# Kernel optimization log

Hardware: AMD Instinct MI355X
Metric: run time of the kernel (lower is better)

## Reference

```python
import jax, jax.numpy as jnp
import numpy as np

D_MODEL = 1024
N_HEADS = 16
LN_EPS = 1e-6  # flax LayerNorm default

def setup_inputs() -> dict:
    key = jax.random.key(0)
    k1, k2, k3 = jax.random.split(key, 3)
    B, S = 2, 2048
    x = jax.random.normal(k1, (B, S, D_MODEL), dtype=jnp.float32)
    W_qkv = jax.random.normal(k2, (D_MODEL, 3 * D_MODEL), dtype=jnp.float32) / np.sqrt(D_MODEL)
    W_out = jax.random.normal(k3, (D_MODEL, D_MODEL), dtype=jnp.float32) / np.sqrt(D_MODEL)
    q_scale = jnp.ones((D_MODEL,), dtype=jnp.float32)
    k_scale = jnp.ones((D_MODEL,), dtype=jnp.float32)
    return {"x": x, "W_qkv": W_qkv, "q_scale": q_scale, "k_scale": k_scale, "W_out": W_out}

def _layernorm(t, scale):
    mu = jnp.mean(t, axis=-1, keepdims=True)
    var = jnp.var(t, axis=-1, keepdims=True)
    return (t - mu) * jax.lax.rsqrt(var + LN_EPS) * scale

def reference(x, W_qkv, q_scale, k_scale, W_out):
    B, S, D = x.shape
    H = N_HEADS
    Hd = D // H
    # fused QKV projection (no bias)
    qkv = jnp.einsum('bsd,de->bse', x, W_qkv)
    q, k, v = jnp.split(qkv, 3, axis=-1)
    # QK-LayerNorm over full d_model (before head split), scale only
    q = _layernorm(q, q_scale)
    k = _layernorm(k, k_scale)
    # split heads: [b, s, h, hd]
    q = q.reshape(B, S, H, Hd)
    k = k.reshape(B, S, H, Hd)
    v = v.reshape(B, S, H, Hd)
    # eager attention with causal mask
    scores = jnp.einsum('bshd,bthd->bhst', q / jnp.sqrt(Hd).astype(q.dtype), k)  # [b,h,s,t]
    future = jnp.triu(jnp.ones((S, S), dtype=bool), 1)  # True on strictly-future positions
    scores = jnp.where(future[None, None, :, :], jnp.finfo(scores.dtype).min, scores)
    attn = jax.nn.softmax(scores, axis=-1)
    ctx = jnp.einsum('bhst,bthd->bshd', attn, v)
    out = jnp.einsum('bsd,de->bse', ctx.reshape(B, S, D), W_out)
    return out
```

## Files before the change

kernel.cpp:

```cpp
#include <hip/hip_runtime.h>
#include <cstdint>
#include <cstddef>

typedef __attribute__((ext_vector_type(8))) short short8;
typedef __attribute__((ext_vector_type(4))) float floatx4;

__device__ __forceinline__ float bf2f(unsigned short u) {
  union { unsigned int i; float f; } c; c.i = ((unsigned int)u) << 16; return c.f;
}
__device__ __forceinline__ unsigned short f2bf(float f) {
  union { float f; unsigned int i; } c; c.f = f;
  unsigned int r = c.i + 0x7fffu + ((c.i >> 16) & 1u);
  return (unsigned short)(r >> 16);
}
__device__ __forceinline__ unsigned short f2bf_trunc(float f) {
  union { float f; unsigned int i; } c; c.f = f;
  return (unsigned short)(c.i >> 16);
}

__device__ __forceinline__ void glds16(const unsigned short* g, unsigned short* l) {
  __builtin_amdgcn_global_load_lds((const __attribute__((address_space(1))) void*)g,
                                   (__attribute__((address_space(3))) void*)l, 16, 0, 0);
}

__global__ __launch_bounds__(256) void k_cvt(const float* __restrict__ in,
                                             unsigned short* __restrict__ out, int n4) {
  int i = blockIdx.x * 256 + threadIdx.x;
  if (i >= n4) return;
  float4 v = ((const float4*)in)[i];
  ushort4 o = { f2bf(v.x), f2bf(v.y), f2bf(v.z), f2bf(v.w) };
  ((ushort4*)out)[i] = o;
}

__global__ __launch_bounds__(1024) void k_transpose_cvt(const float* __restrict__ in,
                                                        unsigned short* __restrict__ out,
                                                        int R, int C) {
  __shared__ unsigned short t[32][33];
  int c = blockIdx.x * 32 + threadIdx.x;
  int r = blockIdx.y * 32 + threadIdx.y;
  t[threadIdx.y][threadIdx.x] = f2bf(in[(size_t)r * C + c]);
  __syncthreads();
  int oc = blockIdx.y * 32 + threadIdx.x;
  int orow = blockIdx.x * 32 + threadIdx.y;
  out[(size_t)orow * R + oc] = t[threadIdx.x][threadIdx.y];
}

__global__ __launch_bounds__(1024) void k_transpose_v(const unsigned short* __restrict__ qkv,
                                                      unsigned short* __restrict__ VT) {
  int bh = blockIdx.z, b = bh >> 4, h = bh & 15;
  __shared__ unsigned short t[32][33];
  int hd = blockIdx.x * 32 + threadIdx.x;
  int s  = blockIdx.y * 32 + threadIdx.y;
  t[threadIdx.y][threadIdx.x] = qkv[(size_t)(b * 2048 + s) * 3072 + 2048 + h * 64 + hd];
  __syncthreads();
  int os  = blockIdx.y * 32 + threadIdx.x;
  int ohd = blockIdx.x * 32 + threadIdx.y;
  VT[((size_t)bh * 64 + ohd) * 2048 + os] = t[threadIdx.x][threadIdx.y];
}

template <int MT, bool F32OUT>
__global__ __launch_bounds__(256) void k_gemm_bt(const unsigned short* __restrict__ A,
                                                 const unsigned short* __restrict__ BT,
                                                 void* __restrict__ Cout,
                                                 int M, int N, int K) {
  constexpr int NI = MT / 32;
  __shared__ unsigned short As[MT * 32];
  __shared__ unsigned short Bs[128 * 32];
  const int bm = blockIdx.x * MT, bn = blockIdx.y * 128;
  const int tid = threadIdx.x;
  const int wave = tid >> 6, lane = tid & 63;
  const int wm = (wave & 1) * (MT / 2), wn = (wave >> 1) * 64;
  const int lrow = lane & 15, lgrp = lane >> 4;
  floatx4 acc[NI][4] = {};

  const int lr4 = lane >> 2, lc8 = (lane & 3) * 8;
  const int br0 = wave * 32;
  const unsigned short* Bg0 = BT + (size_t)(bn + br0 + lr4) * K + lc8;
  const unsigned short* Bg1 = BT + (size_t)(bn + br0 + 16 + lr4) * K + lc8;
  unsigned short* lB0 = &Bs[br0 * 32];
  unsigned short* lB1 = &Bs[(br0 + 16) * 32];
  const int ar0 = wave * (MT / 4);
  const unsigned short* Ag0 = A + (size_t)(bm + ar0 + lr4) * K + lc8;
  const unsigned short* Ag1 = A + (size_t)(bm + ar0 + 16 + lr4) * K + lc8;
  unsigned short* lA0 = &As[ar0 * 32];
  unsigned short* lA1 = &As[(ar0 + 16) * 32];

  for (int k0 = 0; k0 < K; k0 += 32) {
    glds16(Ag0 + k0, lA0);
    if (MT == 128) glds16(Ag1 + k0, lA1);
    glds16(Bg0 + k0, lB0);
    glds16(Bg1 + k0, lB1);
    __syncthreads();
    short8 a[NI], bfr[4];
#pragma unroll
    for (int i = 0; i < NI; ++i)
      a[i] = *(const short8*)&As[(wm + i * 16 + lrow) * 32 + lgrp * 8];
#pragma unroll
    for (int j = 0; j < 4; ++j)
      bfr[j] = *(const short8*)&Bs[(wn + j * 16 + lrow) * 32 + lgrp * 8];
#pragma unroll
    for (int i = 0; i < NI; ++i)
#pragma unroll
      for (int j = 0; j < 4; ++j)
        acc[i][j] = __builtin_amdgcn_mfma_f32_16x16x32_bf16(a[i], bfr[j], acc[i][j], 0, 0, 0);
    __syncthreads();
  }
#pragma unroll
  for (int i = 0; i < NI; ++i)
#pragma unroll
    for (int j = 0; j < 4; ++j)
#pragma unroll
      for (int r = 0; r < 4; ++r) {
        int m = bm + wm + i * 16 + lgrp * 4 + r;
        int n = bn + wn + j * 16 + lrow;
        if (F32OUT)
          ((float*)Cout)[(size_t)m * N + n] = acc[i][j][r];
        else
          ((unsigned short*)Cout)[(size_t)m * N + n] = f2bf(acc[i][j][r]);
      }
}

__global__ __launch_bounds__(256) void k_ln(const unsigned short* __restrict__ qkv,
                                            const float* __restrict__ q_scale,
                                            const float* __restrict__ k_scale,
                                            unsigned short* __restrict__ q_n,
                                            unsigned short* __restrict__ k_n) {
  const int tok = blockIdx.x;
  const int tid = threadIdx.x, wave = tid >> 6, lane = tid & 63;
  __shared__ float red[2][4];
  const unsigned short* row = qkv + (size_t)tok * 3072;
#pragma unroll
  for (int seg = 0; seg < 2; ++seg) {
    const unsigned short* p  = row + seg * 1024;
    const float* sc = seg ? k_scale : q_scale;
    unsigned short* outp = (seg ? k_n : q_n) + (size_t)tok * 1024;
    ushort4 u = *(const ushort4*)&p[tid * 4];
    float xv[4] = { bf2f(u.x), bf2f(u.y), bf2f(u.z), bf2f(u.w) };
    float sum = xv[0] + xv[1] + xv[2] + xv[3];
    float sq  = xv[0]*xv[0] + xv[1]*xv[1] + xv[2]*xv[2] + xv[3]*xv[3];
    for (int off = 32; off; off >>= 1) {
      sum += __shfl_down(sum, off, 64);
      sq  += __shfl_down(sq,  off, 64);
    }
    if (lane == 0) { red[0][wave] = sum; red[1][wave] = sq; }
    __syncthreads();
    sum = red[0][0] + red[0][1] + red[0][2] + red[0][3];
    sq  = red[1][0] + red[1][1] + red[1][2] + red[1][3];
    __syncthreads();
    float mean = sum * (1.0f / 1024.0f);
    float var  = sq * (1.0f / 1024.0f) - mean * mean;
    float rstd = rsqrtf(var + 1e-6f);
    if (seg == 0) rstd *= 0.18033688011112042f;
    float4 su = *(const float4*)&sc[tid * 4];
    ushort4 o;
    o.x = f2bf((xv[0] - mean) * rstd * su.x);
    o.y = f2bf((xv[1] - mean) * rstd * su.y);
    o.z = f2bf((xv[2] - mean) * rstd * su.z);
    o.w = f2bf((xv[3] - mean) * rstd * su.w);
    *(ushort4*)&outp[tid * 4] = o;
  }
}

template <int TB, bool MASKED>
__device__ __forceinline__ void attn_tile(int t0, int q0w,
    const short8 qa0, const short8 qa1,
    const unsigned short* Ks, const unsigned short* Vs, unsigned short* Psw,
    floatx4 (&o)[4], float (&l_i)[4], int lrow, int lgrp) {
  floatx4 sc[TB];
#pragma unroll
  for (int tb = 0; tb < TB; ++tb) {
    floatx4 z = {};
    short8 kb0 = *(const short8*)&Ks[(tb * 16 + lrow) * 72 + lgrp * 8];
    z = __builtin_amdgcn_mfma_f32_16x16x32_bf16(qa0, kb0, z, 0, 0, 0);
    short8 kb1 = *(const short8*)&Ks[(tb * 16 + lrow) * 72 + 32 + lgrp * 8];
    z = __builtin_amdgcn_mfma_f32_16x16x32_bf16(qa1, kb1, z, 0, 0, 0);
    sc[tb] = z;
  }
#pragma unroll
  for (int r = 0; r < 4; ++r) {
    const int qr = q0w + lgrp * 4 + r;
#pragma unroll
    for (int tb = 0; tb < TB; ++tb) {
      float p = exp2f(sc[tb][r]);
      if (MASKED) p = (t0 + tb * 16 + lrow <= qr) ? p : 0.0f;
      unsigned short us = f2bf_trunc(p);
      l_i[r] += bf2f(us);
      Psw[(lgrp * 4 + r) * 136 + tb * 16 + lrow] = us;
    }
  }
#pragma unroll
  for (int kk = 0; kk < TB / 2; ++kk) {
    short8 pa = *(const short8*)&Psw[lrow * 136 + kk * 32 + lgrp * 8];
#pragma unroll
    for (int nb = 0; nb < 4; ++nb) {
      short8 vb = *(const short8*)&Vs[(nb * 16 + lrow) * 136 + kk * 32 + lgrp * 8];
      o[nb] = __builtin_amdgcn_mfma_f32_16x16x32_bf16(pa, vb, o[nb], 0, 0, 0);
    }
  }
}

__global__ __launch_bounds__(256) void k_flash(const unsigned short* __restrict__ q_n,
                                               const unsigned short* __restrict__ k_n,
                                               const unsigned short* __restrict__ VT,
                                               unsigned short* __restrict__ ctx) {
  const int S = 2048, D = 1024;
  const int bh = blockIdx.x, b = bh >> 4, h = bh & 15;
  const int qt = 31 - (int)blockIdx.y;
  const int q0 = qt * 64;
  const int tid = threadIdx.x, wave = tid >> 6, lane = tid & 63;
  const int lrow = lane & 15, lgrp = lane >> 4;
  __shared__ unsigned short Ks[128 * 72];
  __shared__ unsigned short Vs[64 * 136];
  __shared__ unsigned short Ps[4][16 * 136];
  unsigned short* Psw = Ps[wave];

  const unsigned short* kg = k_n + (size_t)(b * S) * D + h * 64;
  const unsigned short* vg = VT + (size_t)bh * 64 * S;
  const int ksr = tid >> 3, ksc = (tid & 7) * 8;
  const int vsr = tid >> 4, vsc = (tid & 15) * 8;

  const int q0w = q0 + wave * 16;
  const unsigned short* qp = q_n + (size_t)(b * S + q0w + lrow) * D + h * 64;
  const short8 qa0 = *(const short8*)(qp + lgrp * 8);
  const short8 qa1 = *(const short8*)(qp + 32 + lgrp * 8);
  floatx4 o[4] = {};
  float l_i[4] = {};

  const int tend = q0 + 64;
  for (int t0 = 0; t0 < tend; t0 += 128) {
#pragma unroll
    for (int j = 0; j < 4; ++j) {
      int r = ksr + j * 32;
      *(int4*)&Ks[r * 72 + ksc] = *(const int4*)(kg + (size_t)(t0 + r) * D + ksc);
    }
#pragma unroll
    for (int j = 0; j < 4; ++j) {
      int r = vsr + j * 16;
      *(int4*)&Vs[r * 136 + vsc] = *(const int4*)(vg + (size_t)r * S + t0 + vsc);
    }
    __syncthreads();
    if (t0 + 128 <= q0)
      attn_tile<8, false>(t0, q0w, qa0, qa1, Ks, Vs, Psw, o, l_i, lrow, lgrp);
    else if (tend - t0 >= 128)
      attn_tile<8, true>(t0, q0w, qa0, qa1, Ks, Vs, Psw, o, l_i, lrow, lgrp);
    else
      attn_tile<4, true>(t0, q0w, qa0, qa1, Ks, Vs, Psw, o, l_i, lrow, lgrp);
    __syncthreads();
  }

  float inv[4];
#pragma unroll
  for (int r = 0; r < 4; ++r) {
    float l = l_i[r];
#pragma unroll
    for (int off = 1; off < 16; off <<= 1) l += __shfl_xor(l, off, 64);
    inv[r] = 1.0f / l;
  }
  unsigned short* op = ctx + (size_t)(b * S + q0w) * D + h * 64;
#pragma unroll
  for (int nb = 0; nb < 4; ++nb)
#pragma unroll
    for (int r = 0; r < 4; ++r) {
      int row = lgrp * 4 + r;
      op[(size_t)row * D + nb * 16 + lrow] = f2bf(o[nb][r] * inv[r]);
    }
}

extern "C" void kernel_launch(void* const* d_in, const int* in_sizes, int n_in,
                              void* d_out, int out_size, void* d_ws, size_t ws_size,
                              hipStream_t stream) {
  const float* x       = (const float*)d_in[0];
  const float* W_qkv   = (const float*)d_in[1];
  const float* q_scale = (const float*)d_in[2];
  const float* k_scale = (const float*)d_in[3];
  const float* W_out   = (const float*)d_in[4];
  float* out = (float*)d_out;
  char* ws = (char*)d_ws;
  unsigned short* WT_qkv = (unsigned short*)(ws + 0);
  unsigned short* WT_out = (unsigned short*)(ws + 6291456);
  unsigned short* qkv    = (unsigned short*)(ws + 8388608);
  unsigned short* q_nb   = (unsigned short*)(ws + 33554432);
  unsigned short* k_nb   = (unsigned short*)(ws + 41943040);
  unsigned short* VT     = (unsigned short*)(ws + 50331648);
  unsigned short* x_bf   = (unsigned short*)(ws + 58720256);
  unsigned short* ctx    = qkv;

  k_cvt<<<4096, 256, 0, stream>>>(x, x_bf, 4096 * 1024 / 4);
  k_transpose_cvt<<<dim3(96, 32), dim3(32, 32), 0, stream>>>(W_qkv, WT_qkv, 1024, 3072);
  k_transpose_cvt<<<dim3(32, 32), dim3(32, 32), 0, stream>>>(W_out, WT_out, 1024, 1024);
  k_gemm_bt<128, false><<<dim3(32, 24), 256, 0, stream>>>(x_bf, WT_qkv, qkv, 4096, 3072, 1024);
  k_ln<<<4096, 256, 0, stream>>>(qkv, q_scale, k_scale, q_nb, k_nb);
  k_transpose_v<<<dim3(2, 64, 32), dim3(32, 32), 0, stream>>>(qkv, VT);
  k_flash<<<dim3(32, 32), 256, 0, stream>>>(q_nb, k_nb, VT, ctx);
  k_gemm_bt<64, true><<<dim3(64, 8), 256, 0, stream>>>(ctx, WT_out, out, 4096, 1024, 1024);
}
```

Baseline: 208.8 us.

## Merge prep and LN/V-transpose launches; transpose score MFMA in flash attention

Three preprocessing kernels (x conversion and two weight transposes) become one k_prep launch, and the LayerNorm and V-transpose kernels become one k_lnv launch. The transposes now use 256-thread blocks instead of 1024. In flash attention, the QK^T MFMA operands are swapped so each lane holds four key positions for a single query. This allows vectorized ushort4 stores of P, a single running row sum with a shorter shuffle reduction, and round-to-nearest instead of truncation when converting P to bf16. The row sum now accumulates the unrounded fp32 p values while the stored P is rounded, which slightly changes numerics.

```diff
diff --git a/kernel.cpp b/kernel.cpp
--- a/kernel.cpp
+++ b/kernel.cpp
@@ -13,49 +13,46 @@
   unsigned int r = c.i + 0x7fffu + ((c.i >> 16) & 1u);
   return (unsigned short)(r >> 16);
 }
-__device__ __forceinline__ unsigned short f2bf_trunc(float f) {
-  union { float f; unsigned int i; } c; c.f = f;
-  return (unsigned short)(c.i >> 16);
-}
 
 __device__ __forceinline__ void glds16(const unsigned short* g, unsigned short* l) {
   __builtin_amdgcn_global_load_lds((const __attribute__((address_space(1))) void*)g,
                                    (__attribute__((address_space(3))) void*)l, 16, 0, 0);
 }
 
-__global__ __launch_bounds__(256) void k_cvt(const float* __restrict__ in,
-                                             unsigned short* __restrict__ out, int n4) {
-  int i = blockIdx.x * 256 + threadIdx.x;
-  if (i >= n4) return;
-  float4 v = ((const float4*)in)[i];
-  ushort4 o = { f2bf(v.x), f2bf(v.y), f2bf(v.z), f2bf(v.w) };
-  ((ushort4*)out)[i] = o;
-}
-
-__global__ __launch_bounds__(1024) void k_transpose_cvt(const float* __restrict__ in,
-                                                        unsigned short* __restrict__ out,
-                                                        int R, int C) {
+__device__ __forceinline__ void tr_tile(const float* __restrict__ in,
+                                        unsigned short* __restrict__ out,
+                                        int R, int C, int bx, int by, int tid,
+                                        unsigned short (*t)[33]) {
+  const int cx = tid & 31, rl = tid >> 5;
+#pragma unroll
+  for (int i = 0; i < 4; ++i)
+    t[rl + i * 8][cx] = f2bf(in[(size_t)(by * 32 + rl + i * 8) * C + bx * 32 + cx]);
+  __syncthreads();
+  const int oc = by * 32 + cx;
+#pragma unroll
+  for (int i = 0; i < 4; ++i)
+    out[(size_t)(bx * 32 + rl + i * 8) * R + oc] = t[cx][rl + i * 8];
+}
+
+__global__ __launch_bounds__(256) void k_prep(const float* __restrict__ x,
+                                              const float* __restrict__ Wq,
+                                              const float* __restrict__ Wo,
+                                              unsigned short* __restrict__ x_bf,
+                                              unsigned short* __restrict__ WTq,
+                                              unsigned short* __restrict__ WTo) {
   __shared__ unsigned short t[32][33];
-  int c = blockIdx.x * 32 + threadIdx.x;
-  int r = blockIdx.y * 32 + threadIdx.y;
-  t[threadIdx.y][threadIdx.x] = f2bf(in[(size_t)r * C + c]);
-  __syncthreads();
-  int oc = blockIdx.y * 32 + threadIdx.x;
-  int orow = blockIdx.x * 32 + threadIdx.y;
-  out[(size_t)orow * R + oc] = t[threadIdx.x][threadIdx.y];
-}
-
-__global__ __launch_bounds__(1024) void k_transpose_v(const unsigned short* __restrict__ qkv,
-                                                      unsigned short* __restrict__ VT) {
-  int bh = blockIdx.z, b = bh >> 4, h = bh & 15;
-  __shared__ unsigned short t[32][33];
-  int hd = blockIdx.x * 32 + threadIdx.x;
-  int s  = blockIdx.y * 32 + threadIdx.y;
-  t[threadIdx.y][threadIdx.x] = qkv[(size_t)(b * 2048 + s) * 3072 + 2048 + h * 64 + hd];
-  __syncthreads();
-  int os  = blockIdx.y * 32 + threadIdx.x;
-  int ohd = blockIdx.x * 32 + threadIdx.y;
-  VT[((size_t)bh * 64 + ohd) * 2048 + os] = t[threadIdx.x][threadIdx.y];
+  const int bid = blockIdx.x, tid = threadIdx.x;
+  if (bid < 3072) {
+    tr_tile(Wq, WTq, 1024, 3072, bid % 96, bid / 96, tid, t);
+  } else if (bid < 4096) {
+    int v = bid - 3072;
+    tr_tile(Wo, WTo, 1024, 1024, v & 31, v >> 5, tid, t);
+  } else {
+    int i = (bid - 4096) * 256 + tid;
+    float4 v = ((const float4*)x)[i];
+    ushort4 o = { f2bf(v.x), f2bf(v.y), f2bf(v.z), f2bf(v.w) };
+    ((ushort4*)x_bf)[i] = o;
+  }
 }
 
 template <int MT, bool F32OUT>
@@ -120,73 +117,88 @@
       }
 }
 
-__global__ __launch_bounds__(256) void k_ln(const unsigned short* __restrict__ qkv,
-                                            const float* __restrict__ q_scale,
-                                            const float* __restrict__ k_scale,
-                                            unsigned short* __restrict__ q_n,
-                                            unsigned short* __restrict__ k_n) {
-  const int tok = blockIdx.x;
-  const int tid = threadIdx.x, wave = tid >> 6, lane = tid & 63;
-  __shared__ float red[2][4];
-  const unsigned short* row = qkv + (size_t)tok * 3072;
-#pragma unroll
-  for (int seg = 0; seg < 2; ++seg) {
-    const unsigned short* p  = row + seg * 1024;
-    const float* sc = seg ? k_scale : q_scale;
-    unsigned short* outp = (seg ? k_n : q_n) + (size_t)tok * 1024;
-    ushort4 u = *(const ushort4*)&p[tid * 4];
-    float xv[4] = { bf2f(u.x), bf2f(u.y), bf2f(u.z), bf2f(u.w) };
-    float sum = xv[0] + xv[1] + xv[2] + xv[3];
-    float sq  = xv[0]*xv[0] + xv[1]*xv[1] + xv[2]*xv[2] + xv[3]*xv[3];
-    for (int off = 32; off; off >>= 1) {
-      sum += __shfl_down(sum, off, 64);
-      sq  += __shfl_down(sq,  off, 64);
-    }
-    if (lane == 0) { red[0][wave] = sum; red[1][wave] = sq; }
-    __syncthreads();
-    sum = red[0][0] + red[0][1] + red[0][2] + red[0][3];
-    sq  = red[1][0] + red[1][1] + red[1][2] + red[1][3];
-    __syncthreads();
-    float mean = sum * (1.0f / 1024.0f);
-    float var  = sq * (1.0f / 1024.0f) - mean * mean;
-    float rstd = rsqrtf(var + 1e-6f);
-    if (seg == 0) rstd *= 0.18033688011112042f;
-    float4 su = *(const float4*)&sc[tid * 4];
-    ushort4 o;
-    o.x = f2bf((xv[0] - mean) * rstd * su.x);
-    o.y = f2bf((xv[1] - mean) * rstd * su.y);
-    o.z = f2bf((xv[2] - mean) * rstd * su.z);
-    o.w = f2bf((xv[3] - mean) * rstd * su.w);
-    *(ushort4*)&outp[tid * 4] = o;
+__global__ __launch_bounds__(256) void k_lnv(const unsigned short* __restrict__ qkv,
+                                             const float* __restrict__ q_scale,
+                                             const float* __restrict__ k_scale,
+                                             unsigned short* __restrict__ q_n,
+                                             unsigned short* __restrict__ k_n,
+                                             unsigned short* __restrict__ VT) {
+  const int bid = blockIdx.x, tid = threadIdx.x;
+  if (bid < 4096) {
+    const int tok = bid;
+    const int wave = tid >> 6, lane = tid & 63;
+    __shared__ float red[2][4];
+    const unsigned short* row = qkv + (size_t)tok * 3072;
+#pragma unroll
+    for (int seg = 0; seg < 2; ++seg) {
+      const unsigned short* p  = row + seg * 1024;
+      const float* sc = seg ? k_scale : q_scale;
+      unsigned short* outp = (seg ? k_n : q_n) + (size_t)tok * 1024;
+      ushort4 u = *(const ushort4*)&p[tid * 4];
+      float xv[4] = { bf2f(u.x), bf2f(u.y), bf2f(u.z), bf2f(u.w) };
+      float sum = xv[0] + xv[1] + xv[2] + xv[3];
+      float sq  = xv[0]*xv[0] + xv[1]*xv[1] + xv[2]*xv[2] + xv[3]*xv[3];
+      for (int off = 32; off; off >>= 1) {
+        sum += __shfl_down(sum, off, 64);
+        sq  += __shfl_down(sq,  off, 64);
+      }
+      if (lane == 0) { red[0][wave] = sum; red[1][wave] = sq; }
+      __syncthreads();
+      sum = red[0][0] + red[0][1] + red[0][2] + red[0][3];
+      sq  = red[1][0] + red[1][1] + red[1][2] + red[1][3];
+      __syncthreads();
+      float mean = sum * (1.0f / 1024.0f);
+      float var  = sq * (1.0f / 1024.0f) - mean * mean;
+      float rstd = rsqrtf(var + 1e-6f);
+      if (seg == 0) rstd *= 0.18033688011112042f;
+      float4 su = *(const float4*)&sc[tid * 4];
+      ushort4 o;
+      o.x = f2bf((xv[0] - mean) * rstd * su.x);
+      o.y = f2bf((xv[1] - mean) * rstd * su.y);
+      o.z = f2bf((xv[2] - mean) * rstd * su.z);
+      o.w = f2bf((xv[3] - mean) * rstd * su.w);
+      *(ushort4*)&outp[tid * 4] = o;
+    }
+  } else {
+    __shared__ unsigned short t[32][33];
+    const int v = bid - 4096;
+    const int bh = v & 31, b = bh >> 4, h = bh & 15;
+    const int sy = (v >> 5) & 63, hx = v >> 11;
+    const int cx = tid & 31, rl = tid >> 5;
+#pragma unroll
+    for (int i = 0; i < 4; ++i)
+      t[rl + i * 8][cx] =
+        qkv[(size_t)(b * 2048 + sy * 32 + rl + i * 8) * 3072 + 2048 + h * 64 + hx * 32 + cx];
+    __syncthreads();
+#pragma unroll
+    for (int i = 0; i < 4; ++i)
+      VT[((size_t)bh * 64 + hx * 32 + rl + i * 8) * 2048 + sy * 32 + cx] = t[cx][rl + i * 8];
   }
 }
 
 template <int TB, bool MASKED>
-__device__ __forceinline__ void attn_tile(int t0, int q0w,
+__device__ __forceinline__ void attn_tile(int t0, int qcol,
     const short8 qa0, const short8 qa1,
     const unsigned short* Ks, const unsigned short* Vs, unsigned short* Psw,
-    floatx4 (&o)[4], float (&l_i)[4], int lrow, int lgrp) {
-  floatx4 sc[TB];
+    floatx4 (&o)[4], float& lsum, int lrow, int lgrp) {
 #pragma unroll
   for (int tb = 0; tb < TB; ++tb) {
-    floatx4 z = {};
+    floatx4 st = {};
     short8 kb0 = *(const short8*)&Ks[(tb * 16 + lrow) * 72 + lgrp * 8];
-    z = __builtin_amdgcn_mfma_f32_16x16x32_bf16(qa0, kb0, z, 0, 0, 0);
+    st = __builtin_amdgcn_mfma_f32_16x16x32_bf16(kb0, qa0, st, 0, 0, 0);
     short8 kb1 = *(const short8*)&Ks[(tb * 16 + lrow) * 72 + 32 + lgrp * 8];
-    z = __builtin_amdgcn_mfma_f32_16x16x32_bf16(qa1, kb1, z, 0, 0, 0);
-    sc[tb] = z;
-  }
-#pragma unroll
-  for (int r = 0; r < 4; ++r) {
-    const int qr = q0w + lgrp * 4 + r;
-#pragma unroll
-    for (int tb = 0; tb < TB; ++tb) {
-      float p = exp2f(sc[tb][r]);
-      if (MASKED) p = (t0 + tb * 16 + lrow <= qr) ? p : 0.0f;
-      unsigned short us = f2bf_trunc(p);
-      l_i[r] += bf2f(us);
-      Psw[(lgrp * 4 + r) * 136 + tb * 16 + lrow] = us;
-    }
+    st = __builtin_amdgcn_mfma_f32_16x16x32_bf16(kb1, qa1, st, 0, 0, 0);
+    ushort4 pu;
+    float ps = 0.0f;
+#pragma unroll
+    for (int r = 0; r < 4; ++r) {
+      float p = exp2f(st[r]);
+      if (MASKED) p = (t0 + tb * 16 + lgrp * 4 + r <= qcol) ? p : 0.0f;
+      ps += p;
+      ((unsigned short*)&pu)[r] = f2bf(p);
+    }
+    lsum += ps;
+    *(ushort4*)&Psw[lrow * 136 + tb * 16 + lgrp * 4] = pu;
   }
 #pragma unroll
   for (int kk = 0; kk < TB / 2; ++kk) {
@@ -220,11 +232,12 @@
   const int vsr = tid >> 4, vsc = (tid & 15) * 8;
 
   const int q0w = q0 + wave * 16;
-  const unsigned short* qp = q_n + (size_t)(b * S + q0w + lrow) * D + h * 64;
+  const int qcol = q0w + lrow;
+  const unsigned short* qp = q_n + (size_t)(b * S + qcol) * D + h * 64;
   const short8 qa0 = *(const short8*)(qp + lgrp * 8);
   const short8 qa1 = *(const short8*)(qp + 32 + lgrp * 8);
   floatx4 o[4] = {};
-  float l_i[4] = {};
+  float lsum = 0.0f;
 
   const int tend = q0 + 64;
   for (int t0 = 0; t0 < tend; t0 += 128) {
@@ -240,22 +253,20 @@
     }
     __syncthreads();
     if (t0 + 128 <= q0)
-      attn_tile<8, false>(t0, q0w, qa0, qa1, Ks, Vs, Psw, o, l_i, lrow, lgrp);
+      attn_tile<8, false>(t0, qcol, qa0, qa1, Ks, Vs, Psw, o, lsum, lrow, lgrp);
     else if (tend - t0 >= 128)
-      attn_tile<8, true>(t0, q0w, qa0, qa1, Ks, Vs, Psw, o, l_i, lrow, lgrp);
+      attn_tile<8, true>(t0, qcol, qa0, qa1, Ks, Vs, Psw, o, lsum, lrow, lgrp);
     else
-      attn_tile<4, true>(t0, q0w, qa0, qa1, Ks, Vs, Psw, o, l_i, lrow, lgrp);
-    __syncthreads();
-  }
-
+      attn_tile<4, true>(t0, qcol, qa0, qa1, Ks, Vs, Psw, o, lsum, lrow, lgrp);
+    __syncthreads();
+  }
+
+  lsum += __shfl_xor(lsum, 16, 64);
+  lsum += __shfl_xor(lsum, 32, 64);
   float inv[4];
 #pragma unroll
-  for (int r = 0; r < 4; ++r) {
-    float l = l_i[r];
-#pragma unroll
-    for (int off = 1; off < 16; off <<= 1) l += __shfl_xor(l, off, 64);
-    inv[r] = 1.0f / l;
-  }
+  for (int r = 0; r < 4; ++r)
+    inv[r] = 1.0f / __shfl(lsum, lgrp * 20 + r, 64);
   unsigned short* op = ctx + (size_t)(b * S + q0w) * D + h * 64;
 #pragma unroll
   for (int nb = 0; nb < 4; ++nb)
@@ -285,12 +296,9 @@
   unsigned short* x_bf   = (unsigned short*)(ws + 58720256);
   unsigned short* ctx    = qkv;
 
-  k_cvt<<<4096, 256, 0, stream>>>(x, x_bf, 4096 * 1024 / 4);
-  k_transpose_cvt<<<dim3(96, 32), dim3(32, 32), 0, stream>>>(W_qkv, WT_qkv, 1024, 3072);
-  k_transpose_cvt<<<dim3(32, 32), dim3(32, 32), 0, stream>>>(W_out, WT_out, 1024, 1024);
+  k_prep<<<8192, 256, 0, stream>>>(x, W_qkv, W_out, x_bf, WT_qkv, WT_out);
   k_gemm_bt<128, false><<<dim3(32, 24), 256, 0, stream>>>(x_bf, WT_qkv, qkv, 4096, 3072, 1024);
-  k_ln<<<4096, 256, 0, stream>>>(qkv, q_scale, k_scale, q_nb, k_nb);
-  k_transpose_v<<<dim3(2, 64, 32), dim3(32, 32), 0, stream>>>(qkv, VT);
+  k_lnv<<<8192, 256, 0, stream>>>(qkv, q_scale, k_scale, q_nb, k_nb, VT);
   k_flash<<<dim3(32, 32), 256, 0, stream>>>(q_nb, k_nb, VT, ctx);
   k_gemm_bt<64, true><<<dim3(64, 8), 256, 0, stream>>>(ctx, WT_out, out, 4096, 1024, 1024);
 }
```

Measured after the change: 191.8 us. 8.1% less time.
